# Performance work log

Measured on AMD Instinct MI355X. Metric: run time of the kernel, lower is better.

Reference implementation:

```python
import jax, jax.numpy as jnp
import numpy as np

N = 2048  # num_nodes (perfect binary tree, heap on nodes 1..N-1, root = node 1)
B = 2048  # batch of independent (phase1, phase2) pairs


def _build_tree(n):
    # left[j]/right[j] hold the compliance SLOT of node j's heap children (2j, 2j+1).
    # Slot of node j is n - j (body loop writes compliance[:, i] at step i with j = n - i).
    left = -np.ones(n, dtype=np.int32)
    right = -np.ones(n, dtype=np.int32)
    for j in range(1, n // 2):
        left[j] = n - 2 * j
        right[j] = n - (2 * j + 1)
    return jnp.array(left), jnp.array(right)


def setup_inputs() -> dict:
    key = jax.random.key(0)
    k1, k2, k3, k4, k5, k6, k7 = jax.random.split(key, 7)

    def make_phase(kd, ko):
        # SPD-ish compliance vectors [d0, o0, o1, d1, o2, d2]: diag in [1,2], off-diag small
        diag = 1.0 + jax.random.uniform(kd, (B, 3))
        off = 0.2 * (jax.random.uniform(ko, (B, 3)) - 0.5)
        return jnp.stack([diag[:, 0], off[:, 0], off[:, 1], diag[:, 1], off[:, 2], diag[:, 2]], axis=-1)

    phase1 = make_phase(k1, k2)
    phase2 = make_phase(k3, k4)
    theta = 0.5 * jax.random.normal(k5, (N,), dtype=jnp.float32)
    activation = jax.random.normal(k6, (N,), dtype=jnp.float32)
    weight = jnp.zeros((N,), dtype=jnp.float32)
    fractions = 0.05 + jax.random.uniform(k7, (N,), dtype=jnp.float32)
    left, right = _build_tree(N)
    return {"phase1": phase1, "phase2": phase2, "theta": theta, "activation": activation,
            "weight": weight, "fractions": fractions, "left": left, "right": right}


def _rot(theta):
    c = jnp.cos(theta)
    s = jnp.sin(theta)
    r2 = jnp.sqrt(jnp.asarray(2.0, theta.dtype))
    return jnp.array([[c * c, s * s, r2 * c * s],
                      [s * s, c * c, -r2 * c * s],
                      [-r2 * s * c, r2 * s * c, c * c - s * s]])


def _rotate_b(v, theta):
    # v: [B,6] Mandel vector -> [B,3,3] -> R(-t) @ M @ R(t) -> [B,6]
    M = jnp.stack([
        jnp.stack([v[:, 0], v[:, 1], v[:, 2]], -1),
        jnp.stack([v[:, 1], v[:, 3], v[:, 4]], -1),
        jnp.stack([v[:, 2], v[:, 4], v[:, 5]], -1)], -2)
    Rm = _rot(theta)
    Rn = _rot(-theta)
    D = jnp.einsum('ij,bjk,kl->bil', Rn, M, Rm)
    return jnp.stack([D[:, 0, 0], D[:, 0, 1], D[:, 0, 2], D[:, 1, 1], D[:, 1, 2], D[:, 2, 2]], -1)


def _homogenise_b(D1, D2, f1, f2):
    # D1, D2: [B,6]; f1, f2 scalars
    gamma = f1 * D2[:, 0] + f2 * D1[:, 0]
    g = jnp.where(gamma == 0, 1.0, gamma)  # guard: only hits discarded leaf-step lanes
    ff = f1 * f2 / g
    d0 = D1[:, 0] * D2[:, 0] / g
    d1 = (f1 * D1[:, 1] * D2[:, 0] + f2 * D2[:, 1] * D1[:, 0]) / g
    d2 = (f1 * D1[:, 2] * D2[:, 0] + f2 * D2[:, 2] * D1[:, 0]) / g
    d3 = f1 * D1[:, 3] + f2 * D2[:, 3] - ff * (D1[:, 1] - D2[:, 1]) ** 2
    d4 = f1 * D1[:, 4] + f2 * D2[:, 4] - ff * (D1[:, 2] - D2[:, 2]) * (D1[:, 1] - D2[:, 1])
    d5 = f1 * D1[:, 5] + f2 * D2[:, 5] - ff * (D1[:, 2] - D2[:, 2]) ** 2
    return jnp.stack([d0, d1, d2, d3, d4, d5], -1)


def _forward(phase1, phase2, theta, fractions, left, right):
    n = theta.shape[0]
    b = phase1.shape[0]

    def step(compliance, i):
        j = n - i                      # node processed at step i (original clamps OOB gathers)
        jj = jnp.minimum(j, n - 1)     # emulate jax's OOB-index clamping at j == n
        l = left[jj]
        r = right[jj]
        is_leaf = (l == -1) & (r == -1)
        # jnp dynamic indexing wraps negative indices: -1 -> n-1
        lw = jnp.where(l < 0, l + n, l)
        rw = jnp.where(r < 0, r + n, r)
        D1 = compliance[:, lw]
        D2 = compliance[:, rw]
        Dh = _homogenise_b(D1, D2, fractions[lw], fractions[rw])
        base = jnp.where((j % 2) == 0, phase1, phase2)  # leaf parity uses unclamped j
        val = jnp.where(is_leaf, base, Dh)
        out = _rotate_b(val, theta[jj])
        return compliance.at[:, i].set(out), None

    compliance = jnp.zeros((b, n, 6), dtype=phase1.dtype)
    compliance, _ = jax.lax.scan(step, compliance, jnp.arange(n))
    return compliance[:, -1]


def reference(phase1, phase2, theta, activation, weight, fractions, left, right):
    n = theta.shape[0]

    # Faithful replication of the original's weight/fraction propagation loops.
    # Note: as in the source, body_fun reads self.fractions (not the propagated fs),
    # so these loops do NOT affect the output (dead code, DCE'd under jit).
    def prop_w(i, ws):
        j = jnp.minimum(n - i, n - 1)
        l = left[j]
        r = right[j]
        is_leaf = (l == -1) & (r == -1)
        upd = jnp.where(is_leaf, jnp.maximum(activation[j], 0.0), ws[l] + ws[r])
        return ws.at[j].set(upd)

    ws = jax.lax.fori_loop(0, n + 1, prop_w, weight)

    def prop_f(i, fs):
        j = jnp.minimum(n - i, n - 1)
        l = left[j]
        r = right[j]
        is_leaf = (l == -1) & (r == -1)
        upd = jnp.where(is_leaf, 0.0, ws[l] / ws[j])
        fs = fs.at[l].set(upd)
        return fs.at[r].set(upd)

    _fs = jax.lax.fori_loop(5, n + 1, prop_f, fractions)  # unused, matching the source

    return _forward(phase1, phase2, theta, fractions, left, right)
```

## Files before the change

### kernel.cpp

```cpp
#include <hip/hip_runtime.h>


#define N_NODES 2048

__device__ __forceinline__ void rotate6(const float* m, float4 r, float* o) {
    float a = r.x, bb = r.y, d = r.z, e = r.w;
    float T00 = m[0]*a  + m[1]*bb - m[2]*d;
    float T01 = m[0]*bb + m[1]*a  + m[2]*d;
    float T02 = (m[0]-m[1])*d + m[2]*e;
    float T10 = m[1]*a  + m[3]*bb - m[4]*d;
    float T11 = m[1]*bb + m[3]*a  + m[4]*d;
    float T12 = (m[1]-m[3])*d + m[4]*e;
    float T20 = m[2]*a  + m[4]*bb - m[5]*d;
    float T21 = m[2]*bb + m[4]*a  + m[5]*d;
    float T22 = (m[2]-m[4])*d + m[5]*e;
    o[0] = a*T00 + bb*T10 - d*T20;
    o[1] = a*T01 + bb*T11 - d*T21;
    o[2] = a*T02 + bb*T12 - d*T22;
    o[3] = bb*T01 + a*T11 + d*T21;
    o[4] = bb*T02 + a*T12 + d*T22;
    o[5] = (T02 - T12)*d + e*T22;
}

__device__ __forceinline__ void homog6(const float* D1, const float* D2,
                                       float f1, float f2, float* o) {
    float gamma = f1*D2[0] + f2*D1[0];
    float g = (gamma == 0.0f) ? 1.0f : gamma;
    float rg = 1.0f / g;
    float ff = f1*f2*rg;
    o[0] = D1[0]*D2[0]*rg;
    o[1] = (f1*D1[1]*D2[0] + f2*D2[1]*D1[0])*rg;
    o[2] = (f1*D1[2]*D2[0] + f2*D2[2]*D1[0])*rg;
    float t1 = D1[1]-D2[1];
    float t2 = D1[2]-D2[2];
    o[3] = f1*D1[3] + f2*D2[3] - ff*t1*t1;
    o[4] = f1*D1[4] + f2*D2[4] - ff*t2*t1;
    o[5] = f1*D1[5] + f2*D2[5] - ff*t2*t2;
}

__device__ __forceinline__ void subtree9(const float* p1, const float* p2,
                                         const float4* __restrict__ rot,
                                         const float2* __restrict__ fr,
                                         int j9, float* outD) {
    float L[6], R[6], H[6];
    rotate6(p1, rot[2*j9],   L);
    rotate6(p2, rot[2*j9+1], R);
    float2 f = fr[j9];
    homog6(L, R, f.x, f.y, H);
    rotate6(H, rot[j9], outD);
}

__device__ __forceinline__ void node8(const float* p1, const float* p2,
                                      const float4* __restrict__ rot,
                                      const float2* __restrict__ fr,
                                      int j8, float* outD) {
    float A[6], B[6], H[6];
    subtree9(p1, p2, rot, fr, 2*j8,   A);
    subtree9(p1, p2, rot, fr, 2*j8+1, B);
    float2 f = fr[j8];
    homog6(A, B, f.x, f.y, H);
    rotate6(H, rot[j8], outD);
}

__global__ void setup_kernel(const float* __restrict__ theta,
                             const float* __restrict__ fractions,
                             float4* __restrict__ rot, float2* __restrict__ fr) {
    int j = blockIdx.x * blockDim.x + threadIdx.x;
    if (j >= 1 && j < N_NODES) {
        float t = theta[j];
        float c = cosf(t), s = sinf(t);
        float a = c*c, bb = s*s;
        float d = sqrtf(2.0f) * c * s;
        rot[j] = make_float4(a, bb, d, a - bb);
    }
    if (j >= 1 && j < N_NODES/2) {
        fr[j] = make_float2(fractions[N_NODES - 2*j], fractions[N_NODES - 2*j - 1]);
    }
}

__global__ __launch_bounds__(256, 4) void tree_kernel(
    const float* __restrict__ phase1, const float* __restrict__ phase2,
    const float4* __restrict__ rot, const float2* __restrict__ fr,
    float* __restrict__ out)
{
    const int tid  = threadIdx.x;
    const int wid  = tid >> 6;
    const int lane = tid & 63;
    const int half = wid & 1;
    const int bloc = wid >> 1;
    const int b    = blockIdx.x * 2 + bloc;

    float p1[6], p2[6];
#pragma unroll
    for (int k = 0; k < 6; ++k) { p1[k] = phase1[b*6+k]; p2[k] = phase2[b*6+k]; }

    float A[6], Bv[6], H[6], v[6];
    {
        int j7 = 128 + half*64 + lane;
        node8(p1, p2, rot, fr, 2*j7,   A);
        node8(p1, p2, rot, fr, 2*j7+1, Bv);
        float2 f = fr[j7];
        homog6(A, Bv, f.x, f.y, H);
        rotate6(H, rot[j7], v);
    }

    int jbase = 128 + half*64;
    int width = 64;
#pragma unroll
    for (int s = 0; s < 6; ++s) {
        float ce[6], co[6];
#pragma unroll
        for (int k = 0; k < 6; ++k) {
            ce[k] = __shfl(v[k], 2*lane,     64);
            co[k] = __shfl(v[k], 2*lane + 1, 64);
        }
        jbase >>= 1;
        width >>= 1;
        if (lane < width) {
            int j = jbase + lane;
            float2 f = fr[j];
            homog6(ce, co, f.x, f.y, H);
            rotate6(H, rot[j], v);
        }
    }

    __shared__ float comb[2][2][6];
    if (lane == 0) {
#pragma unroll
        for (int k = 0; k < 6; ++k) comb[bloc][half][k] = v[k];
    }
    __syncthreads();

    if (tid < 2) {
        float D1[6], D2[6], Hh[6], Dn[6];
#pragma unroll
        for (int k = 0; k < 6; ++k) { D1[k] = comb[tid][0][k]; D2[k] = comb[tid][1][k]; }
        float2 f = fr[1];
        homog6(D1, D2, f.x, f.y, Hh);
        rotate6(Hh, rot[1], Dn);
        int bb = blockIdx.x * 2 + tid;
#pragma unroll
        for (int k = 0; k < 6; ++k) out[bb*6 + k] = Dn[k];
    }
}

extern "C" void kernel_launch(void* const* d_in, const int* in_sizes, int n_in,
                              void* d_out, int out_size, void* d_ws, size_t ws_size,
                              hipStream_t stream) {
    const float* phase1    = (const float*)d_in[0];
    const float* phase2    = (const float*)d_in[1];
    const float* theta     = (const float*)d_in[2];
    const float* fractions = (const float*)d_in[5];
    float* out = (float*)d_out;

    const int B = in_sizes[0] / 6;

    float4* rot = (float4*)d_ws;
    float2* fr  = (float2*)((char*)d_ws + N_NODES * sizeof(float4));

    hipLaunchKernelGGL(setup_kernel, dim3((N_NODES + 255) / 256), dim3(256), 0, stream,
                       theta, fractions, rot, fr);
    hipLaunchKernelGGL(tree_kernel, dim3(B / 2), dim3(256), 0, stream,
                       phase1, phase2, rot, fr, out);
}
```

Before: 83.53 us.

## Precompute structure-of-arrays rotation tables for coalesced leaf-subtree loads

The setup kernel now also writes per-lane rotation and fraction tables laid out as [op][lane], so the leaf-level subtree evaluation in the tree kernel reads consecutive addresses across lanes instead of strided heap indices. The change also swaps the division in homog6 for a hardware reciprocal and drops the occupancy hint from launch_bounds. It costs extra setup work and workspace, and the approximate reciprocal may alter precision slightly.

```diff
diff --git a/kernel.cpp b/kernel.cpp
--- a/kernel.cpp
+++ b/kernel.cpp
@@ -26,7 +26,7 @@
                                        float f1, float f2, float* o) {
     float gamma = f1*D2[0] + f2*D1[0];
     float g = (gamma == 0.0f) ? 1.0f : gamma;
-    float rg = 1.0f / g;
+    float rg = __builtin_amdgcn_rcpf(g);
     float ff = f1*f2*rg;
     o[0] = D1[0]*D2[0]*rg;
     o[1] = (f1*D1[1]*D2[0] + f2*D2[1]*D1[0])*rg;
@@ -38,49 +38,58 @@
     o[5] = f1*D1[5] + f2*D2[5] - ff*t2*t2;
 }
 
-__device__ __forceinline__ void subtree9(const float* p1, const float* p2,
-                                         const float4* __restrict__ rot,
-                                         const float2* __restrict__ fr,
-                                         int j9, float* outD) {
+
+__device__ __forceinline__ void subtree9_s(const float* p1, const float* p2,
+                                           const float4* __restrict__ rotS,
+                                           const float2* __restrict__ frS,
+                                           int p, int ro, int fo, float* outD) {
     float L[6], R[6], H[6];
-    rotate6(p1, rot[2*j9],   L);
-    rotate6(p2, rot[2*j9+1], R);
-    float2 f = fr[j9];
+    rotate6(p1, rotS[(ro+0)*128 + p], L);
+    rotate6(p2, rotS[(ro+1)*128 + p], R);
+    float2 f = frS[fo*128 + p];
     homog6(L, R, f.x, f.y, H);
-    rotate6(H, rot[j9], outD);
+    rotate6(H, rotS[(ro+2)*128 + p], outD);
 }
 
-__device__ __forceinline__ void node8(const float* p1, const float* p2,
-                                      const float4* __restrict__ rot,
-                                      const float2* __restrict__ fr,
-                                      int j8, float* outD) {
-    float A[6], B[6], H[6];
-    subtree9(p1, p2, rot, fr, 2*j8,   A);
-    subtree9(p1, p2, rot, fr, 2*j8+1, B);
-    float2 f = fr[j8];
-    homog6(A, B, f.x, f.y, H);
-    rotate6(H, rot[j8], outD);
+__device__ __forceinline__ float4 mk_rot(float t) {
+    float c = cosf(t), s = sinf(t);
+    float a = c*c, bb = s*s;
+    float d = sqrtf(2.0f) * c * s;
+    return make_float4(a, bb, d, a - bb);
+}
+
+__device__ __forceinline__ float2 mk_fr(const float* fractions, int j) {
+    return make_float2(fractions[N_NODES - 2*j], fractions[N_NODES - 2*j - 1]);
 }
 
 __global__ void setup_kernel(const float* __restrict__ theta,
                              const float* __restrict__ fractions,
-                             float4* __restrict__ rot, float2* __restrict__ fr) {
-    int j = blockIdx.x * blockDim.x + threadIdx.x;
-    if (j >= 1 && j < N_NODES) {
-        float t = theta[j];
-        float c = cosf(t), s = sinf(t);
-        float a = c*c, bb = s*s;
-        float d = sqrtf(2.0f) * c * s;
-        rot[j] = make_float4(a, bb, d, a - bb);
-    }
-    if (j >= 1 && j < N_NODES/2) {
-        fr[j] = make_float2(fractions[N_NODES - 2*j], fractions[N_NODES - 2*j - 1]);
+                             float4* __restrict__ rot, float2* __restrict__ fr,
+                             float4* __restrict__ rotS, float2* __restrict__ frS) {
+    int gid = blockIdx.x * blockDim.x + threadIdx.x;
+    if (gid < N_NODES) {
+        int j = gid;
+        if (j >= 1) rot[j] = mk_rot(theta[j]);
+        if (j >= 1 && j < N_NODES/2) fr[j] = mk_fr(fractions, j);
+    } else {
+        int p = gid - N_NODES;
+        if (p < 128) {
+            int j7 = 128 + p;
+            const int rops[15] = {8*j7, 8*j7+1, 4*j7,  8*j7+2, 8*j7+3, 4*j7+1,  2*j7,
+                                  8*j7+4, 8*j7+5, 4*j7+2,  8*j7+6, 8*j7+7, 4*j7+3,  2*j7+1,  j7};
+            const int fops[7]  = {4*j7, 4*j7+1, 2*j7, 4*j7+2, 4*j7+3, 2*j7+1, j7};
+#pragma unroll
+            for (int op = 0; op < 15; ++op) rotS[op*128 + p] = mk_rot(theta[rops[op]]);
+#pragma unroll
+            for (int op = 0; op < 7; ++op)  frS[op*128 + p]  = mk_fr(fractions, fops[op]);
+        }
     }
 }
 
-__global__ __launch_bounds__(256, 4) void tree_kernel(
+__global__ __launch_bounds__(256) void tree_kernel(
     const float* __restrict__ phase1, const float* __restrict__ phase2,
     const float4* __restrict__ rot, const float2* __restrict__ fr,
+    const float4* __restrict__ rotS, const float2* __restrict__ frS,
     float* __restrict__ out)
 {
     const int tid  = threadIdx.x;
@@ -96,12 +105,23 @@
 
     float A[6], Bv[6], H[6], v[6];
     {
-        int j7 = 128 + half*64 + lane;
-        node8(p1, p2, rot, fr, 2*j7,   A);
-        node8(p1, p2, rot, fr, 2*j7+1, Bv);
-        float2 f = fr[j7];
+        const int p = half*64 + lane;
+        float DA[6], DB[6];
+        subtree9_s(p1, p2, rotS, frS, p, 0, 0, DA);
+        subtree9_s(p1, p2, rotS, frS, p, 3, 1, DB);
+        float2 f = frS[2*128 + p];
+        homog6(DA, DB, f.x, f.y, H);
+        rotate6(H, rotS[6*128 + p], A);
+
+        subtree9_s(p1, p2, rotS, frS, p, 7, 3, DA);
+        subtree9_s(p1, p2, rotS, frS, p, 10, 4, DB);
+        f = frS[5*128 + p];
+        homog6(DA, DB, f.x, f.y, H);
+        rotate6(H, rotS[13*128 + p], Bv);
+
+        f = frS[6*128 + p];
         homog6(A, Bv, f.x, f.y, H);
-        rotate6(H, rot[j7], v);
+        rotate6(H, rotS[14*128 + p], v);
     }
 
     int jbase = 128 + half*64;
@@ -155,11 +175,14 @@
 
     const int B = in_sizes[0] / 6;
 
-    float4* rot = (float4*)d_ws;
-    float2* fr  = (float2*)((char*)d_ws + N_NODES * sizeof(float4));
+    char* ws = (char*)d_ws;
+    float4* rot  = (float4*)ws;                      ws += N_NODES * sizeof(float4);
+    float2* fr   = (float2*)ws;                      ws += (N_NODES/2) * sizeof(float2);
+    float4* rotS = (float4*)ws;                      ws += 15 * 128 * sizeof(float4);
+    float2* frS  = (float2*)ws;
 
-    hipLaunchKernelGGL(setup_kernel, dim3((N_NODES + 255) / 256), dim3(256), 0, stream,
-                       theta, fractions, rot, fr);
+    hipLaunchKernelGGL(setup_kernel, dim3((N_NODES + 128 + 255) / 256), dim3(256), 0, stream,
+                       theta, fractions, rot, fr, rotS, frS);
     hipLaunchKernelGGL(tree_kernel, dim3(B / 2), dim3(256), 0, stream,
-                       phase1, phase2, rot, fr, out);
+                       phase1, phase2, rot, fr, rotS, frS, out);
 }
```

Result: slower. 86.46 us (+3.5%).
